# Kernel tuning notes

Hardware: AMD Instinct MI355X
Metric: run time of the kernel (lower is better)

## Reference

```python
import jax, jax.numpy as jnp
import numpy as np
from jax import lax

T, IMG, C_IN = 2048, 84, 4
HID = 256
NUM_OUT = 18
FEAT = 6 * 6 * 32  # 84 -> 42 -> 21 -> 11 -> 6 with stride-2 SAME convs


def setup_inputs() -> dict:
    key = jax.random.key(0)
    ks = jax.random.split(key, 8)
    d = {}
    d["x"] = jax.random.normal(ks[0], (T, IMG, IMG, C_IN), jnp.float32)
    cin = C_IN
    for i in range(4):
        d[f"conv_w{i}"] = jax.random.normal(ks[1 + i], (3, 3, cin, 32), jnp.float32) * (1.0 / np.sqrt(9 * cin))
        d[f"conv_b{i}"] = jnp.zeros((32,), jnp.float32)
        cin = 32
    d["lstm_w"] = jax.random.normal(ks[5], (FEAT + HID, 4 * HID), jnp.float32) * (1.0 / np.sqrt(FEAT + HID))
    d["lstm_b"] = jnp.zeros((4 * HID,), jnp.float32)
    d["fc_w"] = jax.random.normal(ks[6], (HID, NUM_OUT), jnp.float32) * 0.01
    d["fc_b"] = jnp.zeros((NUM_OUT,), jnp.float32)
    d["c_in"] = jnp.zeros((1, HID), jnp.float32)
    d["h_in"] = jnp.zeros((1, HID), jnp.float32)
    return d


def _conv_stack(x, ws, bs):
    dn = ("NHWC", "HWIO", "NHWC")
    for w, b in zip(ws, bs):
        x = jax.nn.elu(lax.conv_general_dilated(x, w, (2, 2), "SAME", dimension_numbers=dn) + b)
    return x.reshape(x.shape[0], -1)  # [T, FEAT]


def _lstm(feats, c0, h0, lstm_w, lstm_b):
    # BasicLSTMCell: gates [i, j, f, o], forget_bias = 1.0
    def step(carry, xt):
        c, h = carry  # [1, HID] each
        z = jnp.concatenate([xt[None, :], h], axis=1) @ lstm_w + lstm_b
        i, j, f, o = jnp.split(z, 4, axis=1)
        c = c * jax.nn.sigmoid(f + 1.0) + jax.nn.sigmoid(i) * jnp.tanh(j)
        h = jnp.tanh(c) * jax.nn.sigmoid(o)
        return (c, h), h[0]

    (_, _), hs = lax.scan(step, (c0, h0), feats)
    return hs  # [T, HID]


def reference(x, c_in, h_in,
              conv_w0, conv_b0, conv_w1, conv_b1,
              conv_w2, conv_b2, conv_w3, conv_b3,
              lstm_w, lstm_b, fc_w, fc_b):
    feats = _conv_stack(x, [conv_w0, conv_w1, conv_w2, conv_w3],
                        [conv_b0, conv_b1, conv_b2, conv_b3])
    hs = _lstm(feats, c_in, h_in, lstm_w, lstm_b)
    logits = hs @ fc_w + fc_b  # [T, NUM_OUT]
    return logits, hs
```

## Files before the change

kernel.cpp:

```cpp
#include <hip/hip_runtime.h>
#include <hip/hip_bf16.h>

__device__ inline float fsig(float x) { return 1.0f / (1.0f + __expf(-x)); }
__device__ inline float ftanh(float x) {
    float ax = fabsf(x);
    float e = __expf(-2.0f * ax);
    float r = (1.0f - e) / (1.0f + e);
    return x >= 0.0f ? r : -r;
}
__device__ inline float felu(float x) { return x > 0.0f ? x : expm1f(x); }

typedef _Float16 h2_t __attribute__((ext_vector_type(2)));

__device__ inline unsigned int packh2(float a, float b) {
    unsigned short ua = __builtin_bit_cast(unsigned short, (_Float16)a);
    unsigned short ub = __builtin_bit_cast(unsigned short, (_Float16)b);
    return (unsigned int)ua | ((unsigned int)ub << 16);
}
__device__ inline unsigned short f16bits(float a) {
    return __builtin_bit_cast(unsigned short, (_Float16)a);
}

__device__ inline float dot2acc(unsigned int w, unsigned int h, float acc) {
#if __has_builtin(__builtin_amdgcn_fdot2)
    return __builtin_amdgcn_fdot2(__builtin_bit_cast(h2_t, w), __builtin_bit_cast(h2_t, h), acc, false);
#else
    _Float16 wlo = __builtin_bit_cast(_Float16, (unsigned short)(w & 0xffff));
    _Float16 whi = __builtin_bit_cast(_Float16, (unsigned short)(w >> 16));
    _Float16 hlo = __builtin_bit_cast(_Float16, (unsigned short)(h & 0xffff));
    _Float16 hhi = __builtin_bit_cast(_Float16, (unsigned short)(h >> 16));
    return acc + (float)wlo * (float)hlo + (float)whi * (float)hhi;
#endif
}

__global__ __launch_bounds__(256) void conv0_kernel(const float* __restrict__ in,
                                                    const float* __restrict__ wg,
                                                    const float* __restrict__ bias,
                                                    unsigned short* __restrict__ out) {
    constexpr int W = 84, OW = 42, PAD = 0, WP = W + 2;
    __shared__ float in_s[3 * WP * 4];
    constexpr int NQ = 3 * WP;
    const int tid = threadIdx.x;
    const int oy = blockIdx.x;
    const int t = blockIdx.y;
    const int co = tid & 31;

    for (int q = tid; q < NQ; q += 256) {
        int ky = q / WP;
        int col = q - ky * WP;
        int iy = 2 * oy - PAD + ky;
        int ix = col - 1;
        float4 v = make_float4(0.f, 0.f, 0.f, 0.f);
        if (iy >= 0 && iy < W && ix >= 0 && ix < W)
            v = *(const float4*)&in[(((size_t)t * W + iy) * W + ix) * 4];
        *(float4*)&in_s[q * 4] = v;
    }

    float wr[9][4];
#pragma unroll
    for (int tap = 0; tap < 9; ++tap)
#pragma unroll
        for (int j = 0; j < 4; ++j) wr[tap][j] = wg[(tap * 4 + j) * 32 + co];
    __syncthreads();

    const int g = tid >> 5;
    constexpr int NOX = (OW + 7) / 8;
    float acc[NOX];
#pragma unroll
    for (int m = 0; m < NOX; ++m) acc[m] = 0.f;
#pragma unroll
    for (int ky = 0; ky < 3; ++ky)
#pragma unroll
        for (int kx = 0; kx < 3; ++kx) {
            float w0 = wr[ky * 3 + kx][0], w1 = wr[ky * 3 + kx][1];
            float w2 = wr[ky * 3 + kx][2], w3 = wr[ky * 3 + kx][3];
#pragma unroll
            for (int m = 0; m < NOX; ++m) {
                int ox = g + 8 * m;
                if (ox < OW) {
                    int cs = 2 * ox + kx - PAD + 1;
                    float4 xi = *(const float4*)&in_s[(ky * WP + cs) * 4];
                    acc[m] += xi.x * w0 + xi.y * w1 + xi.z * w2 + xi.w * w3;
                }
            }
        }
    float b = bias[co];
#pragma unroll
    for (int m = 0; m < NOX; ++m) {
        int ox = g + 8 * m;
        if (ox < OW)
            out[(((size_t)t * OW + oy) * OW + ox) * 32 + co] = f16bits(felu(acc[m] + b));
    }
}

template <int W, int OW, int PAD, bool F32OUT>
__global__ __launch_bounds__(256) void convh_kernel(const unsigned short* __restrict__ in,
                                                    const float* __restrict__ wg,
                                                    const float* __restrict__ bias,
                                                    void* __restrict__ outv) {
    constexpr int WP = W + 2;
    constexpr int OWH = (OW + 1) / 2;
    __shared__ __align__(16) unsigned short in_s[3][WP][32];
    __shared__ float zs[4][OW * 32];

    const int tid = threadIdx.x;
    const int oy = blockIdx.x;
    const int t = blockIdx.y;
    const int co = tid & 31;
    const int cig = (tid >> 5) & 3;
    const int oxh = tid >> 7;

    constexpr int NQ4 = 3 * WP * 4;
    uint4* in_s4 = reinterpret_cast<uint4*>(&in_s[0][0][0]);
    for (int q = tid; q < NQ4; q += 256) {
        int ky = q / (WP * 4);
        int rem = q - ky * (WP * 4);
        int col = rem >> 2, c4 = rem & 3;
        int iy = 2 * oy - PAD + ky;
        int ix = col - 1;
        uint4 v = make_uint4(0u, 0u, 0u, 0u);
        if (iy >= 0 && iy < W && ix >= 0 && ix < W)
            v = *(const uint4*)&in[(((size_t)t * W + iy) * W + ix) * 32 + c4 * 8];
        in_s4[q] = v;
    }

    unsigned int wr[9][4];
#pragma unroll
    for (int tap = 0; tap < 9; ++tap)
#pragma unroll
        for (int p = 0; p < 4; ++p)
            wr[tap][p] = packh2(wg[(tap * 32 + cig * 8 + 2 * p) * 32 + co],
                                wg[(tap * 32 + cig * 8 + 2 * p + 1) * 32 + co]);
    __syncthreads();

    float acc[OWH];
#pragma unroll
    for (int m = 0; m < OWH; ++m) acc[m] = 0.f;
#pragma unroll
    for (int ky = 0; ky < 3; ++ky)
#pragma unroll
        for (int kx = 0; kx < 3; ++kx) {
            unsigned int w0 = wr[ky * 3 + kx][0], w1 = wr[ky * 3 + kx][1];
            unsigned int w2 = wr[ky * 3 + kx][2], w3 = wr[ky * 3 + kx][3];
#pragma unroll
            for (int m = 0; m < OWH; ++m) {
                int ox = oxh * OWH + m;
                if (ox < OW) {
                    int cs = 2 * ox + kx - PAD + 1;
                    uint4 h8 = *(const uint4*)&in_s[ky][cs][cig * 8];
                    acc[m] = dot2acc(w0, h8.x, acc[m]);
                    acc[m] = dot2acc(w1, h8.y, acc[m]);
                    acc[m] = dot2acc(w2, h8.z, acc[m]);
                    acc[m] = dot2acc(w3, h8.w, acc[m]);
                }
            }
        }
#pragma unroll
    for (int m = 0; m < OWH; ++m) {
        int ox = oxh * OWH + m;
        if (ox < OW) zs[cig][ox * 32 + co] = acc[m];
    }
    __syncthreads();

    for (int idx = tid; idx < OW * 32; idx += 256) {
        float s = zs[0][idx] + zs[1][idx] + zs[2][idx] + zs[3][idx] + bias[idx & 31];
        s = felu(s);
        if constexpr (F32OUT)
            ((float*)outv)[(((size_t)t * OW + oy) * OW) * 32 + idx] = s;
        else
            ((unsigned short*)outv)[(((size_t)t * OW + oy) * OW) * 32 + idx] = f16bits(s);
    }
}

__global__ void gemm_kernel(const float* __restrict__ A, const float* __restrict__ Wx,
                            const float* __restrict__ bias, float* __restrict__ C) {
    __shared__ float As[32][64];
    __shared__ float Bs[32][64];
    const int bn = blockIdx.x, bm = blockIdx.y;
    const int tx = threadIdx.x, ty = threadIdx.y;
    const int tid = ty * 16 + tx;
    float acc[4][4] = {};
    for (int k0 = 0; k0 < 1152; k0 += 32) {
        {
            int r = tid >> 3;
            int c = (tid & 7) * 4;
            float4 a0 = *(const float4*)&A[(size_t)(bm * 64 + r) * 1152 + k0 + c];
            float4 a1 = *(const float4*)&A[(size_t)(bm * 64 + r + 32) * 1152 + k0 + c];
            As[c + 0][r] = a0.x; As[c + 1][r] = a0.y; As[c + 2][r] = a0.z; As[c + 3][r] = a0.w;
            As[c + 0][r + 32] = a1.x; As[c + 1][r + 32] = a1.y; As[c + 2][r + 32] = a1.z; As[c + 3][r + 32] = a1.w;
            int rb = tid >> 4;
            int cb = (tid & 15) * 4;
            *(float4*)&Bs[rb][cb] = *(const float4*)&Wx[(size_t)(k0 + rb) * 1024 + bn * 64 + cb];
            *(float4*)&Bs[rb + 16][cb] = *(const float4*)&Wx[(size_t)(k0 + rb + 16) * 1024 + bn * 64 + cb];
        }
        __syncthreads();
#pragma unroll
        for (int kk = 0; kk < 32; ++kk) {
            float4 a = *(float4*)&As[kk][ty * 4];
            float4 b = *(float4*)&Bs[kk][tx * 4];
            acc[0][0] += a.x * b.x; acc[0][1] += a.x * b.y; acc[0][2] += a.x * b.z; acc[0][3] += a.x * b.w;
            acc[1][0] += a.y * b.x; acc[1][1] += a.y * b.y; acc[1][2] += a.y * b.z; acc[1][3] += a.y * b.w;
            acc[2][0] += a.z * b.x; acc[2][1] += a.z * b.y; acc[2][2] += a.z * b.z; acc[2][3] += a.z * b.w;
            acc[3][0] += a.w * b.x; acc[3][1] += a.w * b.y; acc[3][2] += a.w * b.z; acc[3][3] += a.w * b.w;
        }
        __syncthreads();
    }
#pragma unroll
    for (int i = 0; i < 4; ++i) {
        int row = bm * 64 + ty * 4 + i;
#pragma unroll
        for (int j = 0; j < 4; ++j) {
            int col = bn * 64 + tx * 4 + j;
            C[(size_t)row * 1024 + col] = acc[i][j] + bias[col];
        }
    }
}

__global__ __launch_bounds__(512) void lstm9_kernel(const float* __restrict__ lstm_w,
                                                    const float* __restrict__ xpart,
                                                    const float* __restrict__ c_in,
                                                    const float* __restrict__ h_in,
                                                    float* __restrict__ hs_out) {
    __shared__ __align__(16) unsigned int wl[512][52];
    __shared__ __align__(16) unsigned short hpk[2][256];

    const int tid = threadIdx.x;
    const int wv = tid >> 6;
    const int l = tid & 63;
    const int s = l >> 5;
    const int u0 = (wv << 5) + (l & 31);

    for (int q = 0; q < 4; ++q)
        for (int p = 0; p < 12; ++p)
            wl[tid][q * 12 + p] = packh2(
                lstm_w[(size_t)(1152 + 128 * s + 2 * p) * 1024 + (q << 8) + u0],
                lstm_w[(size_t)(1152 + 128 * s + 2 * p + 1) * 1024 + (q << 8) + u0]);
    unsigned int wreg[4][52];
#pragma unroll
    for (int q = 0; q < 4; ++q)
        for (int p = 12; p < 64; ++p)
            wreg[q][p - 12] = packh2(
                lstm_w[(size_t)(1152 + 128 * s + 2 * p) * 1024 + (q << 8) + u0],
                lstm_w[(size_t)(1152 + 128 * s + 2 * p + 1) * 1024 + (q << 8) + u0]);

    float c_state = c_in[u0];
    if (tid < 256) hpk[0][tid] = f16bits(h_in[tid]);
    __syncthreads();

    float xp0 = xpart[u0], xp1 = xpart[256 + u0], xp2 = xpart[512 + u0], xp3 = xpart[768 + u0];

    for (int t = 0; t < 2048; ++t) {
        const int cur = t & 1;
        const uint4* hq = reinterpret_cast<const uint4*>(&hpk[cur][s << 7]);

        float a0 = 0.f, a1 = 0.f, a2 = 0.f, a3 = 0.f;
        {
            uint4 hA = hq[0], hB = hq[1], hC = hq[2];
            uint4 w0a = *(const uint4*)&wl[tid][0];
            uint4 w0b = *(const uint4*)&wl[tid][4];
            uint4 w0c = *(const uint4*)&wl[tid][8];
            a0 = dot2acc(w0a.x, hA.x, a0); a0 = dot2acc(w0a.y, hA.y, a0);
            a0 = dot2acc(w0a.z, hA.z, a0); a0 = dot2acc(w0a.w, hA.w, a0);
            a0 = dot2acc(w0b.x, hB.x, a0); a0 = dot2acc(w0b.y, hB.y, a0);
            a0 = dot2acc(w0b.z, hB.z, a0); a0 = dot2acc(w0b.w, hB.w, a0);
            a0 = dot2acc(w0c.x, hC.x, a0); a0 = dot2acc(w0c.y, hC.y, a0);
            a0 = dot2acc(w0c.z, hC.z, a0); a0 = dot2acc(w0c.w, hC.w, a0);
            uint4 w1a = *(const uint4*)&wl[tid][12];
            uint4 w1b = *(const uint4*)&wl[tid][16];
            uint4 w1c = *(const uint4*)&wl[tid][20];
            a1 = dot2acc(w1a.x, hA.x, a1); a1 = dot2acc(w1a.y, hA.y, a1);
            a1 = dot2acc(w1a.z, hA.z, a1); a1 = dot2acc(w1a.w, hA.w, a1);
            a1 = dot2acc(w1b.x, hB.x, a1); a1 = dot2acc(w1b.y, hB.y, a1);
            a1 = dot2acc(w1b.z, hB.z, a1); a1 = dot2acc(w1b.w, hB.w, a1);
            a1 = dot2acc(w1c.x, hC.x, a1); a1 = dot2acc(w1c.y, hC.y, a1);
            a1 = dot2acc(w1c.z, hC.z, a1); a1 = dot2acc(w1c.w, hC.w, a1);
            uint4 w2a = *(const uint4*)&wl[tid][24];
            uint4 w2b = *(const uint4*)&wl[tid][28];
            uint4 w2c = *(const uint4*)&wl[tid][32];
            a2 = dot2acc(w2a.x, hA.x, a2); a2 = dot2acc(w2a.y, hA.y, a2);
            a2 = dot2acc(w2a.z, hA.z, a2); a2 = dot2acc(w2a.w, hA.w, a2);
            a2 = dot2acc(w2b.x, hB.x, a2); a2 = dot2acc(w2b.y, hB.y, a2);
            a2 = dot2acc(w2b.z, hB.z, a2); a2 = dot2acc(w2b.w, hB.w, a2);
            a2 = dot2acc(w2c.x, hC.x, a2); a2 = dot2acc(w2c.y, hC.y, a2);
            a2 = dot2acc(w2c.z, hC.z, a2); a2 = dot2acc(w2c.w, hC.w, a2);
            uint4 w3a = *(const uint4*)&wl[tid][36];
            uint4 w3b = *(const uint4*)&wl[tid][40];
            uint4 w3c = *(const uint4*)&wl[tid][44];
            a3 = dot2acc(w3a.x, hA.x, a3); a3 = dot2acc(w3a.y, hA.y, a3);
            a3 = dot2acc(w3a.z, hA.z, a3); a3 = dot2acc(w3a.w, hA.w, a3);
            a3 = dot2acc(w3b.x, hB.x, a3); a3 = dot2acc(w3b.y, hB.y, a3);
            a3 = dot2acc(w3b.z, hB.z, a3); a3 = dot2acc(w3b.w, hB.w, a3);
            a3 = dot2acc(w3c.x, hC.x, a3); a3 = dot2acc(w3c.y, hC.y, a3);
            a3 = dot2acc(w3c.z, hC.z, a3); a3 = dot2acc(w3c.w, hC.w, a3);
        }
#pragma unroll
        for (int c = 3; c < 16; ++c) {
            uint4 h4 = hq[c];
            const int r = 4 * (c - 3);
            a0 = dot2acc(wreg[0][r + 0], h4.x, a0); a0 = dot2acc(wreg[0][r + 1], h4.y, a0);
            a0 = dot2acc(wreg[0][r + 2], h4.z, a0); a0 = dot2acc(wreg[0][r + 3], h4.w, a0);
            a1 = dot2acc(wreg[1][r + 0], h4.x, a1); a1 = dot2acc(wreg[1][r + 1], h4.y, a1);
            a1 = dot2acc(wreg[1][r + 2], h4.z, a1); a1 = dot2acc(wreg[1][r + 3], h4.w, a1);
            a2 = dot2acc(wreg[2][r + 0], h4.x, a2); a2 = dot2acc(wreg[2][r + 1], h4.y, a2);
            a2 = dot2acc(wreg[2][r + 2], h4.z, a2); a2 = dot2acc(wreg[2][r + 3], h4.w, a2);
            a3 = dot2acc(wreg[3][r + 0], h4.x, a3); a3 = dot2acc(wreg[3][r + 1], h4.y, a3);
            a3 = dot2acc(wreg[3][r + 2], h4.z, a3); a3 = dot2acc(wreg[3][r + 3], h4.w, a3);
        }

        float xn0 = 0.f, xn1 = 0.f, xn2 = 0.f, xn3 = 0.f;
        if (t + 1 < 2048) {
            const float* xr = &xpart[(size_t)(t + 1) * 1024];
            xn0 = xr[u0]; xn1 = xr[256 + u0]; xn2 = xr[512 + u0]; xn3 = xr[768 + u0];
        }

        float zi = a0 + __shfl_xor(a0, 32, 64) + xp0;
        float zj = a1 + __shfl_xor(a1, 32, 64) + xp1;
        float zf = a2 + __shfl_xor(a2, 32, 64) + xp2;
        float zo = a3 + __shfl_xor(a3, 32, 64) + xp3;

        c_state = c_state * fsig(zf + 1.0f) + fsig(zi) * ftanh(zj);
        float h = ftanh(c_state) * fsig(zo);
        if (s == 0) {
            hs_out[(size_t)t * 256 + u0] = h;
            hpk[cur ^ 1][u0] = f16bits(h);
        }

        asm volatile("s_waitcnt lgkmcnt(0)\n\ts_barrier" ::: "memory");
        xp0 = xn0; xp1 = xn1; xp2 = xn2; xp3 = xn3;
    }
}

__global__ void logits_kernel(const float* __restrict__ hs, const float* __restrict__ fc_w,
                              const float* __restrict__ fc_b, float* __restrict__ out) {
    int idx = blockIdx.x * 256 + threadIdx.x;
    if (idx >= 2048 * 18) return;
    int t = idx / 18, n = idx % 18;
    float acc = fc_b[n];
    const float* hrow = hs + (size_t)t * 256;
#pragma unroll 4
    for (int k = 0; k < 256; ++k) acc += hrow[k] * fc_w[k * 18 + n];
    out[idx] = acc;
}

extern "C" void kernel_launch(void* const* d_in, const int* in_sizes, int n_in,
                              void* d_out, int out_size, void* d_ws, size_t ws_size,
                              hipStream_t stream) {
    const float* x   = (const float*)d_in[0];
    const float* w0  = (const float*)d_in[1];
    const float* b0  = (const float*)d_in[2];
    const float* w1  = (const float*)d_in[3];
    const float* b1  = (const float*)d_in[4];
    const float* w2  = (const float*)d_in[5];
    const float* b2  = (const float*)d_in[6];
    const float* w3  = (const float*)d_in[7];
    const float* b3  = (const float*)d_in[8];
    const float* lw  = (const float*)d_in[9];
    const float* lb  = (const float*)d_in[10];
    const float* fcw = (const float*)d_in[11];
    const float* fcb = (const float*)d_in[12];
    const float* cin = (const float*)d_in[13];
    const float* hin = (const float*)d_in[14];

    float* outp = (float*)d_out;
    float* hs_out = outp + 2048 * 18;

    const size_t FIXED_B = ((size_t)2048 * 1152 + (size_t)2048 * 1024) * 4;
    const size_t PERT_B = ((size_t)56448 + 14112 + 3872) * 2;

    int C = 128;
    const int cands[5] = {2048, 1024, 512, 256, 128};
    for (int i = 0; i < 5; ++i) {
        if (FIXED_B + (size_t)cands[i] * PERT_B <= ws_size) { C = cands[i]; break; }
    }

    float* feats = (float*)d_ws;
    float* xpart = feats + (size_t)2048 * 1152;
    unsigned short* c0buf = (unsigned short*)(xpart + (size_t)2048 * 1024);
    unsigned short* c1buf = c0buf + (size_t)C * 56448;
    unsigned short* c2buf = c1buf + (size_t)C * 14112;

    for (int t0 = 0; t0 < 2048; t0 += C) {
        const float* xin = x + (size_t)t0 * 84 * 84 * 4;
        conv0_kernel<<<dim3(42, C), 256, 0, stream>>>(xin, w0, b0, c0buf);
        convh_kernel<42, 21, 0, false><<<dim3(21, C), 256, 0, stream>>>(c0buf, w1, b1, c1buf);
        convh_kernel<21, 11, 1, false><<<dim3(11, C), 256, 0, stream>>>(c1buf, w2, b2, c2buf);
        convh_kernel<11, 6, 1, true><<<dim3(6, C), 256, 0, stream>>>(c2buf, w3, b3,
                                                                     feats + (size_t)t0 * 1152);
    }

    gemm_kernel<<<dim3(16, 32), dim3(16, 16), 0, stream>>>(feats, lw, lb, xpart);
    lstm9_kernel<<<1, 512, 0, stream>>>(lw, xpart, cin, hin, hs_out);
    logits_kernel<<<144, 256, 0, stream>>>(hs_out, fcw, fcb, outp);
}
```

Before: 4.337 ms.

## Use MFMA fp16 GEMM, restructure LSTM reduction via LDS, widen conv channel tiling

Replaces the scalar fp32 input-projection GEMM with an MFMA 16x16x32 f16 kernel fed by fp16 features and an fp16 transposed copy of the LSTM weights, which a new conversion kernel produces. The last conv layer now writes fp16 output to match. The LSTM kernel splits the hidden reduction across two 256-thread halves and combines partial sums through shared memory with an extra barrier per step, where it previously used wave shuffles. The conv kernels now compute two output channels per thread over quarter-width strips to reuse each input load. Together these aim to cut GEMM cost and conv LDS traffic, at the price of extra fp16 rounding and an additional barrier in the serial LSTM loop.

```diff
diff --git a/kernel.cpp b/kernel.cpp
--- a/kernel.cpp
+++ b/kernel.cpp
@@ -11,6 +11,8 @@
 __device__ inline float felu(float x) { return x > 0.0f ? x : expm1f(x); }
 
 typedef _Float16 h2_t __attribute__((ext_vector_type(2)));
+typedef _Float16 f16x8 __attribute__((ext_vector_type(8)));
+typedef float f32x4 __attribute__((ext_vector_type(4)));
 
 __device__ inline unsigned int packh2(float a, float b) {
     unsigned short ua = __builtin_bit_cast(unsigned short, (_Float16)a);
@@ -31,6 +33,14 @@
     _Float16 hhi = __builtin_bit_cast(_Float16, (unsigned short)(h >> 16));
     return acc + (float)wlo * (float)hlo + (float)whi * (float)hhi;
 #endif
+}
+
+__global__ __launch_bounds__(256) void convert_lwT(const float* __restrict__ lw,
+                                                   unsigned short* __restrict__ lwhT) {
+    int idx = blockIdx.x * 256 + threadIdx.x;
+    if (idx >= 1152 * 1024) return;
+    int k = idx >> 10, n = idx & 1023;
+    lwhT[(size_t)n * 1152 + k] = f16bits(lw[idx]);
 }
 
 __global__ __launch_bounds__(256) void conv0_kernel(const float* __restrict__ in,
@@ -99,16 +109,16 @@
                                                     const float* __restrict__ bias,
                                                     void* __restrict__ outv) {
     constexpr int WP = W + 2;
-    constexpr int OWH = (OW + 1) / 2;
+    constexpr int OWQ = (OW + 3) / 4;
     __shared__ __align__(16) unsigned short in_s[3][WP][32];
     __shared__ float zs[4][OW * 32];
 
     const int tid = threadIdx.x;
     const int oy = blockIdx.x;
     const int t = blockIdx.y;
-    const int co = tid & 31;
-    const int cig = (tid >> 5) & 3;
-    const int oxh = tid >> 7;
+    const int co16 = tid & 15;
+    const int cig = (tid >> 4) & 3;
+    const int oxq = tid >> 6;
 
     constexpr int NQ4 = 3 * WP * 4;
     uint4* in_s4 = reinterpret_cast<uint4*>(&in_s[0][0][0]);
@@ -124,41 +134,50 @@
         in_s4[q] = v;
     }
 
-    unsigned int wr[9][4];
+    unsigned int wr[9][4][2];
 #pragma unroll
     for (int tap = 0; tap < 9; ++tap)
 #pragma unroll
-        for (int p = 0; p < 4; ++p)
-            wr[tap][p] = packh2(wg[(tap * 32 + cig * 8 + 2 * p) * 32 + co],
-                                wg[(tap * 32 + cig * 8 + 2 * p + 1) * 32 + co]);
+        for (int p = 0; p < 4; ++p) {
+            wr[tap][p][0] = packh2(wg[(tap * 32 + cig * 8 + 2 * p) * 32 + co16],
+                                   wg[(tap * 32 + cig * 8 + 2 * p + 1) * 32 + co16]);
+            wr[tap][p][1] = packh2(wg[(tap * 32 + cig * 8 + 2 * p) * 32 + co16 + 16],
+                                   wg[(tap * 32 + cig * 8 + 2 * p + 1) * 32 + co16 + 16]);
+        }
     __syncthreads();
 
-    float acc[OWH];
-#pragma unroll
-    for (int m = 0; m < OWH; ++m) acc[m] = 0.f;
+    float acc0[OWQ], acc1[OWQ];
+#pragma unroll
+    for (int m = 0; m < OWQ; ++m) { acc0[m] = 0.f; acc1[m] = 0.f; }
 #pragma unroll
     for (int ky = 0; ky < 3; ++ky)
 #pragma unroll
         for (int kx = 0; kx < 3; ++kx) {
-            unsigned int w0 = wr[ky * 3 + kx][0], w1 = wr[ky * 3 + kx][1];
-            unsigned int w2 = wr[ky * 3 + kx][2], w3 = wr[ky * 3 + kx][3];
-#pragma unroll
-            for (int m = 0; m < OWH; ++m) {
-                int ox = oxh * OWH + m;
+            const int tap = ky * 3 + kx;
+#pragma unroll
+            for (int m = 0; m < OWQ; ++m) {
+                int ox = oxq * OWQ + m;
                 if (ox < OW) {
                     int cs = 2 * ox + kx - PAD + 1;
                     uint4 h8 = *(const uint4*)&in_s[ky][cs][cig * 8];
-                    acc[m] = dot2acc(w0, h8.x, acc[m]);
-                    acc[m] = dot2acc(w1, h8.y, acc[m]);
-                    acc[m] = dot2acc(w2, h8.z, acc[m]);
-                    acc[m] = dot2acc(w3, h8.w, acc[m]);
+                    acc0[m] = dot2acc(wr[tap][0][0], h8.x, acc0[m]);
+                    acc0[m] = dot2acc(wr[tap][1][0], h8.y, acc0[m]);
+                    acc0[m] = dot2acc(wr[tap][2][0], h8.z, acc0[m]);
+                    acc0[m] = dot2acc(wr[tap][3][0], h8.w, acc0[m]);
+                    acc1[m] = dot2acc(wr[tap][0][1], h8.x, acc1[m]);
+                    acc1[m] = dot2acc(wr[tap][1][1], h8.y, acc1[m]);
+                    acc1[m] = dot2acc(wr[tap][2][1], h8.z, acc1[m]);
+                    acc1[m] = dot2acc(wr[tap][3][1], h8.w, acc1[m]);
                 }
             }
         }
 #pragma unroll
-    for (int m = 0; m < OWH; ++m) {
-        int ox = oxh * OWH + m;
-        if (ox < OW) zs[cig][ox * 32 + co] = acc[m];
+    for (int m = 0; m < OWQ; ++m) {
+        int ox = oxq * OWQ + m;
+        if (ox < OW) {
+            zs[cig][ox * 32 + co16] = acc0[m];
+            zs[cig][ox * 32 + co16 + 16] = acc1[m];
+        }
     }
     __syncthreads();
 
@@ -172,86 +191,95 @@
     }
 }
 
-__global__ void gemm_kernel(const float* __restrict__ A, const float* __restrict__ Wx,
-                            const float* __restrict__ bias, float* __restrict__ C) {
-    __shared__ float As[32][64];
-    __shared__ float Bs[32][64];
-    const int bn = blockIdx.x, bm = blockIdx.y;
-    const int tx = threadIdx.x, ty = threadIdx.y;
-    const int tid = ty * 16 + tx;
-    float acc[4][4] = {};
-    for (int k0 = 0; k0 < 1152; k0 += 32) {
-        {
-            int r = tid >> 3;
-            int c = (tid & 7) * 4;
-            float4 a0 = *(const float4*)&A[(size_t)(bm * 64 + r) * 1152 + k0 + c];
-            float4 a1 = *(const float4*)&A[(size_t)(bm * 64 + r + 32) * 1152 + k0 + c];
-            As[c + 0][r] = a0.x; As[c + 1][r] = a0.y; As[c + 2][r] = a0.z; As[c + 3][r] = a0.w;
-            As[c + 0][r + 32] = a1.x; As[c + 1][r + 32] = a1.y; As[c + 2][r + 32] = a1.z; As[c + 3][r + 32] = a1.w;
-            int rb = tid >> 4;
-            int cb = (tid & 15) * 4;
-            *(float4*)&Bs[rb][cb] = *(const float4*)&Wx[(size_t)(k0 + rb) * 1024 + bn * 64 + cb];
-            *(float4*)&Bs[rb + 16][cb] = *(const float4*)&Wx[(size_t)(k0 + rb + 16) * 1024 + bn * 64 + cb];
-        }
-        __syncthreads();
-#pragma unroll
-        for (int kk = 0; kk < 32; ++kk) {
-            float4 a = *(float4*)&As[kk][ty * 4];
-            float4 b = *(float4*)&Bs[kk][tx * 4];
-            acc[0][0] += a.x * b.x; acc[0][1] += a.x * b.y; acc[0][2] += a.x * b.z; acc[0][3] += a.x * b.w;
-            acc[1][0] += a.y * b.x; acc[1][1] += a.y * b.y; acc[1][2] += a.y * b.z; acc[1][3] += a.y * b.w;
-            acc[2][0] += a.z * b.x; acc[2][1] += a.z * b.y; acc[2][2] += a.z * b.z; acc[2][3] += a.z * b.w;
-            acc[3][0] += a.w * b.x; acc[3][1] += a.w * b.y; acc[3][2] += a.w * b.z; acc[3][3] += a.w * b.w;
-        }
-        __syncthreads();
-    }
-#pragma unroll
-    for (int i = 0; i < 4; ++i) {
-        int row = bm * 64 + ty * 4 + i;
-#pragma unroll
-        for (int j = 0; j < 4; ++j) {
-            int col = bn * 64 + tx * 4 + j;
-            C[(size_t)row * 1024 + col] = acc[i][j] + bias[col];
-        }
-    }
-}
-
-__global__ __launch_bounds__(512) void lstm9_kernel(const float* __restrict__ lstm_w,
-                                                    const float* __restrict__ xpart,
-                                                    const float* __restrict__ c_in,
-                                                    const float* __restrict__ h_in,
-                                                    float* __restrict__ hs_out) {
-    __shared__ __align__(16) unsigned int wl[512][52];
-    __shared__ __align__(16) unsigned short hpk[2][256];
-
+__global__ __launch_bounds__(256) void gemm_mfma(const unsigned short* __restrict__ A,
+                                                 const unsigned short* __restrict__ BT,
+                                                 const float* __restrict__ bias,
+                                                 float* __restrict__ C) {
+    __shared__ __align__(16) unsigned short As[64][40];
+    __shared__ __align__(16) unsigned short Bs[64][40];
+    const int bn = blockIdx.x;
+    const int bm = blockIdx.y;
     const int tid = threadIdx.x;
     const int wv = tid >> 6;
     const int l = tid & 63;
-    const int s = l >> 5;
-    const int u0 = (wv << 5) + (l & 31);
+    const int lm = l & 15;
+    const int kg = l >> 4;
+
+    f32x4 acc[4] = {};
+
+    const int sr = tid >> 2;
+    const int sk = (tid & 3) * 8;
+
+    for (int k0 = 0; k0 < 1152; k0 += 32) {
+        *(uint4*)&As[sr][sk] = *(const uint4*)&A[(size_t)(bm * 64 + sr) * 1152 + k0 + sk];
+        *(uint4*)&Bs[sr][sk] = *(const uint4*)&BT[(size_t)(bn * 64 + sr) * 1152 + k0 + sk];
+        __syncthreads();
+
+        f16x8 a = *(const f16x8*)&As[(wv << 4) + lm][kg * 8];
+        f16x8 b0 = *(const f16x8*)&Bs[lm][kg * 8];
+        f16x8 b1 = *(const f16x8*)&Bs[16 + lm][kg * 8];
+        f16x8 b2 = *(const f16x8*)&Bs[32 + lm][kg * 8];
+        f16x8 b3 = *(const f16x8*)&Bs[48 + lm][kg * 8];
+        acc[0] = __builtin_amdgcn_mfma_f32_16x16x32_f16(a, b0, acc[0], 0, 0, 0);
+        acc[1] = __builtin_amdgcn_mfma_f32_16x16x32_f16(a, b1, acc[1], 0, 0, 0);
+        acc[2] = __builtin_amdgcn_mfma_f32_16x16x32_f16(a, b2, acc[2], 0, 0, 0);
+        acc[3] = __builtin_amdgcn_mfma_f32_16x16x32_f16(a, b3, acc[3], 0, 0, 0);
+        __syncthreads();
+    }
+
+#pragma unroll
+    for (int nt = 0; nt < 4; ++nt) {
+        int col = bn * 64 + nt * 16 + lm;
+        float bv = bias[col];
+#pragma unroll
+        for (int j = 0; j < 4; ++j) {
+            int row = bm * 64 + (wv << 4) + kg * 4 + j;
+            C[(size_t)row * 1024 + col] = acc[nt][j] + bv;
+        }
+    }
+}
+
+__global__ __attribute__((amdgpu_flat_work_group_size(512, 512)))
+void lstm7_kernel(const float* __restrict__ lstm_w,
+                  const float* __restrict__ xpart,
+                  const float* __restrict__ c_in,
+                  const float* __restrict__ h_in,
+                  float* __restrict__ hs_out) {
+    __shared__ __align__(16) unsigned int wl[512][52];
+    __shared__ float zsm[2][4][256];
+    __shared__ __align__(16) unsigned int hpk[2][2][68];
+
+    const int tid = threadIdx.x;
+    const int s = tid >> 8;
+    const int u = tid & 255;
 
     for (int q = 0; q < 4; ++q)
-        for (int p = 0; p < 12; ++p)
-            wl[tid][q * 12 + p] = packh2(
-                lstm_w[(size_t)(1152 + 128 * s + 2 * p) * 1024 + (q << 8) + u0],
-                lstm_w[(size_t)(1152 + 128 * s + 2 * p + 1) * 1024 + (q << 8) + u0]);
+        for (int p = 0; p < 12; ++p) {
+            int gp = 64 * s + p;
+            wl[tid][q * 12 + p] = packh2(lstm_w[(size_t)(1152 + 2 * gp) * 1024 + (q << 8) + u],
+                                         lstm_w[(size_t)(1152 + 2 * gp + 1) * 1024 + (q << 8) + u]);
+        }
     unsigned int wreg[4][52];
 #pragma unroll
     for (int q = 0; q < 4; ++q)
-        for (int p = 12; p < 64; ++p)
-            wreg[q][p - 12] = packh2(
-                lstm_w[(size_t)(1152 + 128 * s + 2 * p) * 1024 + (q << 8) + u0],
-                lstm_w[(size_t)(1152 + 128 * s + 2 * p + 1) * 1024 + (q << 8) + u0]);
-
-    float c_state = c_in[u0];
-    if (tid < 256) hpk[0][tid] = f16bits(h_in[tid]);
+        for (int p = 12; p < 64; ++p) {
+            int gp = 64 * s + p;
+            wreg[q][p - 12] = packh2(lstm_w[(size_t)(1152 + 2 * gp) * 1024 + (q << 8) + u],
+                                     lstm_w[(size_t)(1152 + 2 * gp + 1) * 1024 + (q << 8) + u]);
+        }
+
+    float c_state = c_in[u];
+    if (tid < 256) {
+        unsigned short* hrow = (unsigned short*)&hpk[0][u >> 7][0];
+        hrow[u & 127] = f16bits(h_in[u]);
+    }
     __syncthreads();
 
-    float xp0 = xpart[u0], xp1 = xpart[256 + u0], xp2 = xpart[512 + u0], xp3 = xpart[768 + u0];
+    float xp0 = xpart[u], xp1 = xpart[256 + u], xp2 = xpart[512 + u], xp3 = xpart[768 + u];
 
     for (int t = 0; t < 2048; ++t) {
         const int cur = t & 1;
-        const uint4* hq = reinterpret_cast<const uint4*>(&hpk[cur][s << 7]);
+        const uint4* hq = reinterpret_cast<const uint4*>(&hpk[cur][s][0]);
 
         float a0 = 0.f, a1 = 0.f, a2 = 0.f, a3 = 0.f;
         {
@@ -306,23 +334,29 @@
             a3 = dot2acc(wreg[3][r + 0], h4.x, a3); a3 = dot2acc(wreg[3][r + 1], h4.y, a3);
             a3 = dot2acc(wreg[3][r + 2], h4.z, a3); a3 = dot2acc(wreg[3][r + 3], h4.w, a3);
         }
+        zsm[s][0][u] = a0;
+        zsm[s][1][u] = a1;
+        zsm[s][2][u] = a2;
+        zsm[s][3][u] = a3;
 
         float xn0 = 0.f, xn1 = 0.f, xn2 = 0.f, xn3 = 0.f;
         if (t + 1 < 2048) {
             const float* xr = &xpart[(size_t)(t + 1) * 1024];
-            xn0 = xr[u0]; xn1 = xr[256 + u0]; xn2 = xr[512 + u0]; xn3 = xr[768 + u0];
-        }
-
-        float zi = a0 + __shfl_xor(a0, 32, 64) + xp0;
-        float zj = a1 + __shfl_xor(a1, 32, 64) + xp1;
-        float zf = a2 + __shfl_xor(a2, 32, 64) + xp2;
-        float zo = a3 + __shfl_xor(a3, 32, 64) + xp3;
-
+            xn0 = xr[u]; xn1 = xr[256 + u]; xn2 = xr[512 + u]; xn3 = xr[768 + u];
+        }
+
+        asm volatile("s_waitcnt lgkmcnt(0)\n\ts_barrier" ::: "memory");
+
+        float zi = zsm[0][0][u] + zsm[1][0][u] + xp0;
+        float zj = zsm[0][1][u] + zsm[1][1][u] + xp1;
+        float zf = zsm[0][2][u] + zsm[1][2][u] + xp2;
+        float zo = zsm[0][3][u] + zsm[1][3][u] + xp3;
         c_state = c_state * fsig(zf + 1.0f) + fsig(zi) * ftanh(zj);
         float h = ftanh(c_state) * fsig(zo);
-        if (s == 0) {
-            hs_out[(size_t)t * 256 + u0] = h;
-            hpk[cur ^ 1][u0] = f16bits(h);
+        if (tid < 256) {
+            hs_out[(size_t)t * 256 + u] = h;
+            unsigned short* hrow = (unsigned short*)&hpk[cur ^ 1][u >> 7][0];
+            hrow[u & 127] = f16bits(h);
         }
 
         asm volatile("s_waitcnt lgkmcnt(0)\n\ts_barrier" ::: "memory");
@@ -364,7 +398,13 @@
     float* outp = (float*)d_out;
     float* hs_out = outp + 2048 * 18;
 
-    const size_t FIXED_B = ((size_t)2048 * 1152 + (size_t)2048 * 1024) * 4;
+    float* xpart = (float*)d_ws;
+    unsigned short* feats16 = (unsigned short*)(xpart + (size_t)2048 * 1024);
+    unsigned short* lwhT = feats16 + (size_t)2048 * 1152;
+    unsigned short* bufs = lwhT + (size_t)1024 * 1152;
+
+    const size_t FIXED_B = (size_t)2048 * 1024 * 4 + (size_t)2048 * 1152 * 2 +
+                           (size_t)1024 * 1152 * 2;
     const size_t PERT_B = ((size_t)56448 + 14112 + 3872) * 2;
 
     int C = 128;
@@ -373,22 +413,22 @@
         if (FIXED_B + (size_t)cands[i] * PERT_B <= ws_size) { C = cands[i]; break; }
     }
 
-    float* feats = (float*)d_ws;
-    float* xpart = feats + (size_t)2048 * 1152;
-    unsigned short* c0buf = (unsigned short*)(xpart + (size_t)2048 * 1024);
+    unsigned short* c0buf = bufs;
     unsigned short* c1buf = c0buf + (size_t)C * 56448;
     unsigned short* c2buf = c1buf + (size_t)C * 14112;
+
+    convert_lwT<<<4608, 256, 0, stream>>>(lw, lwhT);
 
     for (int t0 = 0; t0 < 2048; t0 += C) {
         const float* xin = x + (size_t)t0 * 84 * 84 * 4;
         conv0_kernel<<<dim3(42, C), 256, 0, stream>>>(xin, w0, b0, c0buf);
         convh_kernel<42, 21, 0, false><<<dim3(21, C), 256, 0, stream>>>(c0buf, w1, b1, c1buf);
         convh_kernel<21, 11, 1, false><<<dim3(11, C), 256, 0, stream>>>(c1buf, w2, b2, c2buf);
-        convh_kernel<11, 6, 1, true><<<dim3(6, C), 256, 0, stream>>>(c2buf, w3, b3,
-                                                                     feats + (size_t)t0 * 1152);
-    }
-
-    gemm_kernel<<<dim3(16, 32), dim3(16, 16), 0, stream>>>(feats, lw, lb, xpart);
-    lstm9_kernel<<<1, 512, 0, stream>>>(lw, xpart, cin, hin, hs_out);
+        convh_kernel<11, 6, 1, false><<<dim3(6, C), 256, 0, stream>>>(
+            c2buf, w3, b3, feats16 + (size_t)t0 * 1152);
+    }
+
+    gemm_mfma<<<dim3(16, 32), 256, 0, stream>>>(feats16, lwhT, lb, xpart);
+    lstm7_kernel<<<1, 512, 0, stream>>>(lw, xpart, cin, hin, hs_out);
     logits_kernel<<<144, 256, 0, stream>>>(hs_out, fcw, fcb, outp);
 }
```

New measurement: 4.377 ms. Within noise of the previous version (+0.9%).
